# Kernel tuning notes

Hardware: AMD Instinct MI355X
Metric: run time of the kernel (lower is better)

The kernel has to match this reference:

```python
import jax, jax.numpy as jnp
import numpy as np

KERNEL_SIZE = 4     # kernel taps per input pixel
NUM_INTERP = 4      # bilinear -> 4 interpolation points per tap
B, C, IH, IW = 4, 128, 128, 256
OH, OW = 256, 512


def setup_inputs() -> dict:
    key = jax.random.key(0)
    kx, kmx, kmy, kw = jax.random.split(key, 4)
    x = jax.random.normal(kx, (B, C, IH, IW), dtype=jnp.float32)
    # integer interpolation-point coordinates into the (OH, OW) output grid
    map_x = jax.random.randint(kmx, (IH, IW, KERNEL_SIZE, NUM_INTERP, 1), 0, OW, dtype=jnp.int32)
    map_y = jax.random.randint(kmy, (IH, IW, KERNEL_SIZE, NUM_INTERP, 1), 0, OH, dtype=jnp.int32)
    sample_map = jnp.concatenate([map_x, map_y], axis=-1)  # (ih, iw, k, p, 2) -> (x, y)
    # bilinear-style weights, normalized over the interpolation points
    w = jax.random.uniform(kw, (IH, IW, KERNEL_SIZE, NUM_INTERP), dtype=jnp.float32)
    interp_weights = w / jnp.sum(w, axis=-1, keepdims=True)
    return {"x": x, "sample_map": sample_map, "interp_weights": interp_weights,
            "oh": OH, "ow": OW}


def reference(x, sample_map, interp_weights, oh, ow):
    # weighted_mapped_avg_unpool: scatter-add input/kernel_size into the output
    # at each interpolation point, scaled by its interpolation weight.
    b, c, ih, iw = x.shape
    k, p = sample_map.shape[2], sample_map.shape[3]
    n = ih * iw
    xflat = x.reshape(b, c, n)                                      # (B, C, N)
    # flattened output index y*ow + x for every (pixel, tap, interp point)
    idx = (sample_map[..., 1] * ow + sample_map[..., 0]).reshape(n, k * p)
    w = (interp_weights / k).reshape(n, k * p)                      # avg over kernel taps
    out = jnp.zeros((b, c, oh * ow), dtype=x.dtype)
    for t in range(k * p):  # small fixed loop over kernel*interp taps (16)
        out = out.at[:, :, idx[:, t]].add(xflat * w[:, t])
    return out.reshape(b, c, oh, ow)
```

## Files before the change

kernel.cpp:

```cpp
#include <hip/hip_runtime.h>
#include <hip/hip_fp16.h>

#define IHc 128
#define IWc 256
#define OHc 256
#define OWc 512
#define Kc  4
#define Pc  4
#define Bc  4
#define Cc  128

constexpr int Nn  = IHc * IWc;
constexpr int Ee  = Nn * Kc * Pc;
constexpr int Oo  = OHc * OWc;
constexpr int BC  = Bc * Cc;
constexpr int CAP = 24;

typedef float    f32x4 __attribute__((ext_vector_type(4)));
typedef float    f32x2 __attribute__((ext_vector_type(2)));
typedef unsigned u32x4 __attribute__((ext_vector_type(4)));
typedef int      i32x4 __attribute__((ext_vector_type(4)));

static __device__ __forceinline__ unsigned short h_bits(__half h) {
    unsigned short u; __builtin_memcpy(&u, &h, 2); return u;
}
static __device__ __forceinline__ float f_from_hbits(unsigned u) {
    __half h; unsigned short us = (unsigned short)(u & 0xffffu);
    __builtin_memcpy(&h, &us, 2); return __half2float(h);
}
static __device__ __forceinline__ float2 h2_to_f2(unsigned u) {
    __half2 h; __builtin_memcpy(&h, &u, 4); return __half22float2(h);
}


#define TP 64
#define TN 256

__global__ __launch_bounds__(256) void prep_kernel(
        const float* __restrict__ x, __half* __restrict__ xt,
        const i32x4* __restrict__ sm2, const f32x2* __restrict__ iw2,
        int* __restrict__ counts, unsigned* __restrict__ entries) {
    int tid = threadIdx.x;
    int g = (blockIdx.y * gridDim.x + blockIdx.x) * 256 + tid;
    i32x4 e2 = __builtin_nontemporal_load(&sm2[g]);
    f32x2 w2 = __builtin_nontemporal_load(&iw2[g]);
    int n = g >> 3;
    {
        int o = e2.y * OWc + e2.x;
        unsigned ent = ((unsigned)n << 16) |
                       (unsigned)h_bits(__float2half_rn(w2.x * 0.25f));
        int pos = atomicAdd(&counts[o], 1);
        if (pos < CAP) entries[o * CAP + pos] = ent;
    }
    {
        int o = e2.w * OWc + e2.z;
        unsigned ent = ((unsigned)n << 16) |
                       (unsigned)h_bits(__float2half_rn(w2.y * 0.25f));
        int pos = atomicAdd(&counts[o], 1);
        if (pos < CAP) entries[o * CAP + pos] = ent;
    }

    __shared__ __half lds[TP][TN];
    int n0 = blockIdx.x * TN;
    int p0 = blockIdx.y * TP;
    #pragma unroll 8
    for (int i = 0; i < TP; ++i) {
        float v = __builtin_nontemporal_load(&x[(size_t)(p0 + i) * Nn + n0 + tid]);
        lds[i][tid] = __float2half_rn(v);
    }
    __syncthreads();
    alignas(16) __half tmp[TP];
    #pragma unroll
    for (int i = 0; i < TP; ++i) tmp[i] = lds[i][tid];
    f32x4* dst = (f32x4*)(xt + (size_t)(n0 + tid) * BC + p0);
    const f32x4* src = (const f32x4*)tmp;
    #pragma unroll
    for (int q = 0; q < TP / 8; ++q) dst[q] = src[q];
}


#define TILE_O 32
#define TPIT 68

__global__ __launch_bounds__(256) void gather11(const u32x4* __restrict__ xt4,
                                                const int* __restrict__ counts,
                                                const unsigned* __restrict__ entries,
                                                float* __restrict__ out) {
    __shared__ int scnt[TILE_O];
    __shared__ float tbuf[TILE_O][TPIT];

    int tid = threadIdx.x;
    int bid = blockIdx.x;
    int g    = bid & 7;
    int o0   = (bid >> 3) * TILE_O;

    if (tid < TILE_O) {
        int c = counts[o0 + tid];
        scnt[tid] = (c < CAP) ? c : CAP;
    }
    __syncthreads();

    int w = tid >> 6;
    int l = tid & 63;
    int s = l >> 3;
    int q = l & 7;
    const u32x4* __restrict__ xb = xt4 + g * 8 + q;

    int px  = 8 * w + s;
    int js  = (o0 + px) * CAP;
    int cnt = scnt[px];

    float acc[8];
    #pragma unroll
    for (int i = 0; i < 8; ++i) acc[i] = 0.f;

    for (int j = 0; j < cnt; j += 2) {
        unsigned e0 = entries[js + j];
        unsigned e1 = (j + 1 < cnt) ? entries[js + j + 1] : 0u;
        u32x4 r0 = xb[(size_t)(e0 >> 16) * 64];
        u32x4 r1 = xb[(size_t)(e1 >> 16) * 64];
        float w0 = f_from_hbits(e0);
        float w1 = f_from_hbits(e1);
        float2 a0 = h2_to_f2(r0.x), a1 = h2_to_f2(r0.y);
        float2 a2 = h2_to_f2(r0.z), a3 = h2_to_f2(r0.w);
        float2 b0 = h2_to_f2(r1.x), b1 = h2_to_f2(r1.y);
        float2 b2 = h2_to_f2(r1.z), b3 = h2_to_f2(r1.w);
        acc[0] += w0 * a0.x + w1 * b0.x;  acc[1] += w0 * a0.y + w1 * b0.y;
        acc[2] += w0 * a1.x + w1 * b1.x;  acc[3] += w0 * a1.y + w1 * b1.y;
        acc[4] += w0 * a2.x + w1 * b2.x;  acc[5] += w0 * a2.y + w1 * b2.y;
        acc[6] += w0 * a3.x + w1 * b3.x;  acc[7] += w0 * a3.y + w1 * b3.y;
    }

    {
        f32x4 lo = { acc[0], acc[1], acc[2], acc[3] };
        f32x4 hi = { acc[4], acc[5], acc[6], acc[7] };
        float* row = tbuf[px];
        *(f32x4*)(row + 8 * q)     = lo;
        *(f32x4*)(row + 8 * q + 4) = hi;
    }
    __syncthreads();

    {
        int pr = tid >> 2;
        int qt = tid & 3;
        float* base = out + (size_t)(64 * g + pr) * Oo + o0;
        int p0x = 4 * qt;
        f32x4 v0 = { tbuf[p0x + 0][pr], tbuf[p0x + 1][pr],
                     tbuf[p0x + 2][pr], tbuf[p0x + 3][pr] };
        f32x4 v1 = { tbuf[16 + p0x + 0][pr], tbuf[16 + p0x + 1][pr],
                     tbuf[16 + p0x + 2][pr], tbuf[16 + p0x + 3][pr] };
        __builtin_nontemporal_store(v0, (f32x4*)(base + p0x));
        __builtin_nontemporal_store(v1, (f32x4*)(base + 16 + p0x));
    }
}


__global__ void fallback_scatter(const float* __restrict__ x, const int* __restrict__ sm,
                                 const float* __restrict__ iw, float* __restrict__ out) {
    int e = blockIdx.x * blockDim.x + threadIdx.x;
    if (e >= Ee) return;
    int ox = sm[2 * e + 0];
    int oy = sm[2 * e + 1];
    int o = oy * OWc + ox;
    int n = e >> 4;
    float w = iw[e] * 0.25f;
    for (int p = 0; p < BC; ++p)
        atomicAdd(&out[(size_t)p * Oo + o], x[(size_t)p * Nn + n] * w);
}


extern "C" void kernel_launch(void* const* d_in, const int* in_sizes, int n_in,
                              void* d_out, int out_size, void* d_ws, size_t ws_size,
                              hipStream_t stream) {
    const float* x  = (const float*)d_in[0];
    const int*   sm = (const int*)d_in[1];
    const float* iw = (const float*)d_in[2];
    float* out = (float*)d_out;

    constexpr size_t WS_NEED = 13107712 + (size_t)Nn * BC * 2;
    if (ws_size < WS_NEED) {
        (void)hipMemsetAsync(d_out, 0, (size_t)out_size * sizeof(float), stream);
        fallback_scatter<<<Ee / 256, 256, 0, stream>>>(x, sm, iw, out);
        return;
    }

    char* ws = (char*)d_ws;
    int*      counts  = (int*)(ws + 0);
    unsigned* entries = (unsigned*)(ws + 524800);
    __half*   xt      = (__half*)(ws + 13107712);

    (void)hipMemsetAsync(counts, 0, Oo * sizeof(int), stream);

    dim3 tgrid(Nn / TN, BC / TP);
    prep_kernel<<<tgrid, 256, 0, stream>>>(x, xt, (const i32x4*)sm, (const f32x2*)iw,
                                           counts, entries);

    gather11<<<(Oo / TILE_O) * 8, 256, 0, stream>>>((const u32x4*)xt, counts, entries, out);
}
```

Measured before the change: 159.3 us.

## Widen gather tile to two pixels per thread with vectorized entry loads

The gather kernel now uses 512-thread blocks covering 128 output pixels, so each thread accumulates two pixels instead of one. Each pixel's bucket entries are read as one 16-byte vector, and the inner loop is unrolled to four gathers at a time, which puts more independent xt loads in flight per thread. The separate counts preload into shared memory and its barrier are removed, and the transpose/store stage is extended to cover the wider tile. The cost is more registers per thread and a larger shared tile, which may reduce occupancy, and some lanes do wasted work when counts are uneven.

```diff
diff --git a/kernel.cpp b/kernel.cpp
--- a/kernel.cpp
+++ b/kernel.cpp
@@ -79,26 +79,51 @@
 }
 
 
-#define TILE_O 32
+#define TILE_O 128
 #define TPIT 68
 
-__global__ __launch_bounds__(256) void gather11(const u32x4* __restrict__ xt4,
+#define GATHER_PX(acc, cnt, js)                                             \
+    for (int j = 0; j < cnt; j += 4) {                                      \
+        u32x4 es = *(const u32x4*)(entries + js + j);                       \
+        unsigned e0 = es.x;                                                 \
+        unsigned e1 = (j + 1 < cnt) ? es.y : 0u;                            \
+        unsigned e2 = (j + 2 < cnt) ? es.z : 0u;                            \
+        unsigned e3 = (j + 3 < cnt) ? es.w : 0u;                            \
+        u32x4 r0 = xb[(size_t)(e0 >> 16) * 64];                             \
+        u32x4 r1 = xb[(size_t)(e1 >> 16) * 64];                             \
+        u32x4 r2 = xb[(size_t)(e2 >> 16) * 64];                             \
+        u32x4 r3 = xb[(size_t)(e3 >> 16) * 64];                             \
+        float w0 = f_from_hbits(e0), w1 = f_from_hbits(e1);                 \
+        float w2 = f_from_hbits(e2), w3 = f_from_hbits(e3);                 \
+        float2 t0, t1;                                                      \
+        t0 = h2_to_f2(r0.x); t1 = h2_to_f2(r1.x);                           \
+        acc[0] += w0 * t0.x + w1 * t1.x;  acc[1] += w0 * t0.y + w1 * t1.y;  \
+        t0 = h2_to_f2(r0.y); t1 = h2_to_f2(r1.y);                           \
+        acc[2] += w0 * t0.x + w1 * t1.x;  acc[3] += w0 * t0.y + w1 * t1.y;  \
+        t0 = h2_to_f2(r0.z); t1 = h2_to_f2(r1.z);                           \
+        acc[4] += w0 * t0.x + w1 * t1.x;  acc[5] += w0 * t0.y + w1 * t1.y;  \
+        t0 = h2_to_f2(r0.w); t1 = h2_to_f2(r1.w);                           \
+        acc[6] += w0 * t0.x + w1 * t1.x;  acc[7] += w0 * t0.y + w1 * t1.y;  \
+        t0 = h2_to_f2(r2.x); t1 = h2_to_f2(r3.x);                           \
+        acc[0] += w2 * t0.x + w3 * t1.x;  acc[1] += w2 * t0.y + w3 * t1.y;  \
+        t0 = h2_to_f2(r2.y); t1 = h2_to_f2(r3.y);                           \
+        acc[2] += w2 * t0.x + w3 * t1.x;  acc[3] += w2 * t0.y + w3 * t1.y;  \
+        t0 = h2_to_f2(r2.z); t1 = h2_to_f2(r3.z);                           \
+        acc[4] += w2 * t0.x + w3 * t1.x;  acc[5] += w2 * t0.y + w3 * t1.y;  \
+        t0 = h2_to_f2(r2.w); t1 = h2_to_f2(r3.w);                           \
+        acc[6] += w2 * t0.x + w3 * t1.x;  acc[7] += w2 * t0.y + w3 * t1.y;  \
+    }
+
+__global__ __launch_bounds__(512) void gather15(const u32x4* __restrict__ xt4,
                                                 const int* __restrict__ counts,
                                                 const unsigned* __restrict__ entries,
                                                 float* __restrict__ out) {
-    __shared__ int scnt[TILE_O];
     __shared__ float tbuf[TILE_O][TPIT];
 
     int tid = threadIdx.x;
     int bid = blockIdx.x;
     int g    = bid & 7;
     int o0   = (bid >> 3) * TILE_O;
-
-    if (tid < TILE_O) {
-        int c = counts[o0 + tid];
-        scnt[tid] = (c < CAP) ? c : CAP;
-    }
-    __syncthreads();
 
     int w = tid >> 6;
     int l = tid & 63;
@@ -106,51 +131,51 @@
     int q = l & 7;
     const u32x4* __restrict__ xb = xt4 + g * 8 + q;
 
-    int px  = 8 * w + s;
-    int js  = (o0 + px) * CAP;
-    int cnt = scnt[px];
-
-    float acc[8];
+    int pxA = 16 * w + s;
+    int pxB = pxA + 8;
+    int oA  = o0 + pxA;
+    int oB  = o0 + pxB;
+    int cA  = counts[oA];  cA = (cA < CAP) ? cA : CAP;
+    int cB  = counts[oB];  cB = (cB < CAP) ? cB : CAP;
+    int jsA = oA * CAP;
+    int jsB = oB * CAP;
+
+    float accA[8], accB[8];
     #pragma unroll
-    for (int i = 0; i < 8; ++i) acc[i] = 0.f;
-
-    for (int j = 0; j < cnt; j += 2) {
-        unsigned e0 = entries[js + j];
-        unsigned e1 = (j + 1 < cnt) ? entries[js + j + 1] : 0u;
-        u32x4 r0 = xb[(size_t)(e0 >> 16) * 64];
-        u32x4 r1 = xb[(size_t)(e1 >> 16) * 64];
-        float w0 = f_from_hbits(e0);
-        float w1 = f_from_hbits(e1);
-        float2 a0 = h2_to_f2(r0.x), a1 = h2_to_f2(r0.y);
-        float2 a2 = h2_to_f2(r0.z), a3 = h2_to_f2(r0.w);
-        float2 b0 = h2_to_f2(r1.x), b1 = h2_to_f2(r1.y);
-        float2 b2 = h2_to_f2(r1.z), b3 = h2_to_f2(r1.w);
-        acc[0] += w0 * a0.x + w1 * b0.x;  acc[1] += w0 * a0.y + w1 * b0.y;
-        acc[2] += w0 * a1.x + w1 * b1.x;  acc[3] += w0 * a1.y + w1 * b1.y;
-        acc[4] += w0 * a2.x + w1 * b2.x;  acc[5] += w0 * a2.y + w1 * b2.y;
-        acc[6] += w0 * a3.x + w1 * b3.x;  acc[7] += w0 * a3.y + w1 * b3.y;
-    }
-
-    {
-        f32x4 lo = { acc[0], acc[1], acc[2], acc[3] };
-        f32x4 hi = { acc[4], acc[5], acc[6], acc[7] };
-        float* row = tbuf[px];
-        *(f32x4*)(row + 8 * q)     = lo;
-        *(f32x4*)(row + 8 * q + 4) = hi;
+    for (int i = 0; i < 8; ++i) { accA[i] = 0.f; accB[i] = 0.f; }
+
+    GATHER_PX(accA, cA, jsA)
+    GATHER_PX(accB, cB, jsB)
+
+    {
+        float* rowA = tbuf[pxA];
+        f32x4 loA = { accA[0], accA[1], accA[2], accA[3] };
+        f32x4 hiA = { accA[4], accA[5], accA[6], accA[7] };
+        *(f32x4*)(rowA + 8 * q)     = loA;
+        *(f32x4*)(rowA + 8 * q + 4) = hiA;
+        float* rowB = tbuf[pxB];
+        f32x4 loB = { accB[0], accB[1], accB[2], accB[3] };
+        f32x4 hiB = { accB[4], accB[5], accB[6], accB[7] };
+        *(f32x4*)(rowB + 8 * q)     = loB;
+        *(f32x4*)(rowB + 8 * q + 4) = hiB;
     }
     __syncthreads();
 
     {
-        int pr = tid >> 2;
-        int qt = tid & 3;
+        int pr = tid >> 3;
+        int qt = tid & 7;
+        int p0x = 4 * qt;
         float* base = out + (size_t)(64 * g + pr) * Oo + o0;
-        int p0x = 4 * qt;
-        f32x4 v0 = { tbuf[p0x + 0][pr], tbuf[p0x + 1][pr],
-                     tbuf[p0x + 2][pr], tbuf[p0x + 3][pr] };
-        f32x4 v1 = { tbuf[16 + p0x + 0][pr], tbuf[16 + p0x + 1][pr],
-                     tbuf[16 + p0x + 2][pr], tbuf[16 + p0x + 3][pr] };
-        __builtin_nontemporal_store(v0, (f32x4*)(base + p0x));
-        __builtin_nontemporal_store(v1, (f32x4*)(base + 16 + p0x));
+        #pragma unroll
+        for (int h = 0; h < 2; ++h) {
+            int off = 64 * h;
+            f32x4 v0 = { tbuf[off + p0x + 0][pr], tbuf[off + p0x + 1][pr],
+                         tbuf[off + p0x + 2][pr], tbuf[off + p0x + 3][pr] };
+            f32x4 v1 = { tbuf[off + 32 + p0x + 0][pr], tbuf[off + 32 + p0x + 1][pr],
+                         tbuf[off + 32 + p0x + 2][pr], tbuf[off + 32 + p0x + 3][pr] };
+            __builtin_nontemporal_store(v0, (f32x4*)(base + off + p0x));
+            __builtin_nontemporal_store(v1, (f32x4*)(base + off + 32 + p0x));
+        }
     }
 }
 
@@ -195,5 +220,5 @@
     prep_kernel<<<tgrid, 256, 0, stream>>>(x, xt, (const i32x4*)sm, (const f32x2*)iw,
                                            counts, entries);
 
-    gather11<<<(Oo / TILE_O) * 8, 256, 0, stream>>>((const u32x4*)xt, counts, entries, out);
-}
+    gather15<<<(Oo / TILE_O) * 8, 512, 0, stream>>>((const u32x4*)xt, counts, entries, out);
+}
```

Result: faster. 150.2 us (-5.7%).
